# Kernel tuning notes

Measured on AMD Instinct MI355X. Metric: run time of the kernel, lower is better.

The kernel has to match this reference:

```python
import jax, jax.numpy as jnp
import numpy as np

B, C, H, W = 4, 32, 64, 64
K = 3
HEADS = 8
SF = 4
D = C * K * K          # 288, unfold token dim
E = D // 2             # 144, reduced dim
DH = E // HEADS        # 18, head dim
SCALE = DH ** -0.5
N = H * W              # 4096 tokens


def unfold(x):
    # x: (B,C,H,W) -> (B, C*K*K, H*W), torch.nn.Unfold ordering (c, kh, kw)
    xp = jnp.pad(x, ((0, 0), (0, 0), (1, 1), (1, 1)))
    patches = jnp.stack([xp[:, :, i:i + H, j:j + W] for i in range(K) for j in range(K)], axis=2)
    return patches.reshape(x.shape[0], C * K * K, H * W)


def fold(cols):
    # inverse of unfold: scatter-add overlapping patches back, crop padding
    b = cols.shape[0]
    y = cols.reshape(b, C, K, K, H, W)
    out = jnp.zeros((b, C, H + 2, W + 2), cols.dtype)
    for i in range(K):
        for j in range(K):
            out = out.at[:, :, i:i + H, j:j + W].add(y[:, :, i, j])
    return out[:, :, 1:-1, 1:-1]


def layernorm_cols(cols, g, b):
    # LayerNorm over D applied on (B,N,D) view, returned as (B,D,N)
    xt = cols.transpose(0, 2, 1)
    mu = xt.mean(-1, keepdims=True)
    var = xt.var(-1, keepdims=True)
    y = (xt - mu) / jnp.sqrt(var + 1e-5) * g + b
    return y.transpose(0, 2, 1)


def emha(x, wr, br, wqkv, we, be):
    # x: (B, D, N)
    b, _, n_tok = x.shape
    xr = jnp.einsum('bdn,ed->ben', x, wr) + br[None, :, None]   # Conv1d k=1 reduction
    t = xr.transpose(0, 2, 1)                                   # (B,N,E)
    qkv = t @ wqkv.T                                            # Linear, no bias
    q, k, v = jnp.split(qkv, 3, axis=-1)
    n = n_tok // SF

    def rs(a):
        return a.reshape(b, n_tok, HEADS, DH).transpose(0, 2, 1, 3).reshape(b, HEADS, SF, n, DH)

    q, k, v = rs(q), rs(k), rs(v)
    attn = jax.nn.softmax(jnp.einsum('bhsnd,bhsmd->bhsnm', q, k) * SCALE, axis=-1)
    o = jnp.einsum('bhsnm,bhsmd->bhsnd', attn, v)
    o = o.reshape(b, HEADS, n_tok, DH).transpose(0, 2, 1, 3).reshape(b, n_tok, E).transpose(0, 2, 1)
    return jnp.einsum('ben,fe->bfn', o, we) + be[None, :, None]  # Conv1d k=1 expansion


def conv3x3(x, w, b):
    y = jax.lax.conv_general_dilated(x, w, (1, 1), ((1, 1), (1, 1)),
                                     dimension_numbers=('NCHW', 'OIHW', 'NCHW'))
    return y + b[None, :, None, None]


def setup_inputs() -> dict:
    key = jax.random.key(0)
    ks = jax.random.split(key, 20)
    s = 0.02
    inp = {
        'x': jax.random.normal(ks[0], (B, C, H, W), jnp.float32),
        'ln_g': jnp.ones((D,), jnp.float32),
        'ln_b': jnp.zeros((D,), jnp.float32),
        'conv_w': jax.random.normal(ks[1], (C, C, 3, 3), jnp.float32) * s,
        'conv_b': jnp.zeros((C,), jnp.float32),
    }
    for i in range(3):
        k0, k1, k2 = jax.random.split(ks[2 + i], 3)
        inp[f'wr{i+1}'] = jax.random.normal(k0, (E, D), jnp.float32) * s
        inp[f'br{i+1}'] = jnp.zeros((E,), jnp.float32)
        inp[f'wqkv{i+1}'] = jax.random.normal(k1, (3 * E, E), jnp.float32) * s
        inp[f'we{i+1}'] = jax.random.normal(k2, (D, E), jnp.float32) * s
        inp[f'be{i+1}'] = jnp.zeros((D,), jnp.float32)
    return inp


def reference(x, ln_g, ln_b, conv_w, conv_b,
              wr1, br1, wqkv1, we1, be1,
              wr2, br2, wqkv2, we2, be2,
              wr3, br3, wqkv3, we3, be3):
    t = x
    for (wr, br, wqkv, we, be) in ((wr1, br1, wqkv1, we1, be1),
                                   (wr2, br2, wqkv2, we2, be2),
                                   (wr3, br3, wqkv3, we3, be3)):
        cols = unfold(t)
        cols_n = layernorm_cols(cols, ln_g, ln_b)
        cols = emha(cols_n, wr, br, wqkv, we, be) + cols
        t = fold(cols)
    return x + jax.nn.elu(conv3x3(t, conv_w, conv_b))
```

## Files before the change

### kernel.cpp

```cpp
#include <hip/hip_runtime.h>
#include <math.h>

#define BN 4
#define CC 32
#define HH 64
#define WW 64
#define DD 288
#define EE 144
#define NTOK 4096
#define SCALE_F 0.2357022603955158f
#define QSCALE  0.3401074286f
#define QST 192
#define KST 32
#define MQKV 528

typedef __bf16 bf16x8 __attribute__((ext_vector_type(8)));
typedef float floatx4 __attribute__((ext_vector_type(4)));
typedef unsigned short u16x8 __attribute__((ext_vector_type(8)));

__device__ __forceinline__ unsigned short f2bf(float x) {
    unsigned int u = __float_as_uint(x);
    u += 0x7fffu + ((u >> 16) & 1u);
    return (unsigned short)(u >> 16);
}
__device__ __forceinline__ float bf2f(unsigned short s) {
    return __uint_as_float(((unsigned int)s) << 16);
}
__device__ __forceinline__ unsigned int pack_bf_trunc(float a, float b) {
    return __builtin_amdgcn_perm(__float_as_uint(b), __float_as_uint(a), 0x07060302u);
}
__device__ __forceinline__ void plswap32(unsigned int& a, unsigned int& b) {
    asm("v_permlane32_swap_b32 %0, %1" : "+v"(a), "+v"(b));
}
__device__ __forceinline__ void plswap16(unsigned int& a, unsigned int& b) {
    asm("v_permlane16_swap_b32 %0, %1" : "+v"(a), "+v"(b));
}

__global__ __launch_bounds__(256) void setup_k(
    const float* __restrict__ wr0, const float* __restrict__ br0,
    const float* __restrict__ wr1, const float* __restrict__ br1,
    const float* __restrict__ wr2, const float* __restrict__ br2,
    const float* __restrict__ g,  const float* __restrict__ lb,
    const float* __restrict__ wqkv0, const float* __restrict__ wqkv1, const float* __restrict__ wqkv2,
    const float* __restrict__ we0,   const float* __restrict__ we1,   const float* __restrict__ we2,
    unsigned short* __restrict__ wg_bf, float* __restrict__ wgsum, float* __restrict__ wbeta,
    unsigned short* __restrict__ wqkv_bf, unsigned short* __restrict__ we_bf)
{
    int blk = blockIdx.x;
    int tid = threadIdx.x;
    if (blk < 3) {
        if (tid < 144) {
            int l = blk, e = tid;
            const float* wr = (l == 0) ? wr0 : ((l == 1) ? wr1 : wr2);
            const float* br = (l == 0) ? br0 : ((l == 1) ? br1 : br2);
            float sg = 0.f, sb = 0.f;
            for (int d = 0; d < DD; ++d) {
                float w = wr[e * DD + d];
                float wgv = w * g[d];
                wg_bf[((size_t)l * EE + e) * DD + d] = f2bf(wgv);
                sg += wgv;
                sb += w * lb[d];
            }
            wgsum[l * EE + e] = sg;
            wbeta[l * EE + e] = sb + br[e];
        }
        return;
    }
    int idx = (blk - 3) * 256 + tid;
    const int T1 = 3 * MQKV * 160;
    const int T2 = 3 * 288 * 160;
    if (idx < T1) {
        int l = idx / (MQKV * 160), r = idx % (MQKV * 160);
        int m = r / 160, k = r % 160;
        const float* w = (l == 0) ? wqkv0 : ((l == 1) ? wqkv1 : wqkv2);
        float v = 0.f;
        if (k < 144) {
            if (m < 192) {
                int h = m / 24, j = m % 24;
                if (j < 18) v = w[(h * 18 + j) * 144 + k] * QSCALE;
            } else if (m < 384) {
                int mm = m - 192, h = mm / 24, j = mm % 24;
                if (j < 18) v = w[(144 + h * 18 + j) * 144 + k];
            } else {
                v = w[(288 + (m - 384)) * 144 + k];
            }
        }
        wqkv_bf[idx] = f2bf(v);
    } else if (idx < T1 + T2) {
        int j = idx - T1;
        int l = j / (288 * 160), r = j % (288 * 160);
        int m = r / 160, k = r % 160;
        const float* w = (l == 0) ? we0 : ((l == 1) ? we1 : we2);
        we_bf[j] = (k < 144) ? f2bf(w[m * 144 + k]) : 0;
    }
}

__global__ __launch_bounds__(512) void fgemm1_k(
    const float* __restrict__ t, const unsigned short* __restrict__ wg,
    const float* __restrict__ wgsum, const float* __restrict__ wbeta,
    unsigned short* __restrict__ xrT)
{
    __shared__ unsigned short Cs[64 * 296];
    __shared__ float red1[8][64], red2[8][64];
    int tid = threadIdx.x;
    int lane = tid & 63, part = tid >> 6;
    int b = blockIdx.x >> 6, nc = blockIdx.x & 63;
    int w = lane;
    const float* tb = t + (size_t)b * CC * HH * WW;
    __attribute__((aligned(8))) unsigned short loc[36];
    float s1 = 0.f, s2 = 0.f;
    #pragma unroll
    for (int c4 = 0; c4 < 4; ++c4) {
        int c = part * 4 + c4;
        const float* tc = tb + (size_t)c * 4096;
        #pragma unroll
        for (int i = 0; i < 3; ++i) {
            int hr = nc + i - 1;
            bool rok = ((unsigned)hr < 64u);
            #pragma unroll
            for (int j = 0; j < 3; ++j) {
                int wc = w + j - 1;
                bool ok = rok && ((unsigned)wc < 64u);
                float v = ok ? tc[hr * 64 + wc] : 0.f;
                loc[c4 * 9 + i * 3 + j] = f2bf(v);
                s1 += v;
                s2 = fmaf(v, v, s2);
            }
        }
    }
    {
        unsigned short* cr = &Cs[lane * 296 + part * 36];
        #pragma unroll
        for (int k = 0; k < 9; ++k)
            *(unsigned long long*)&cr[k * 4] = *(const unsigned long long*)&loc[k * 4];
    }
    red1[part][lane] = s1;
    red2[part][lane] = s2;
    __syncthreads();
    if (tid < 64) {
        float a = 0.f, q = 0.f;
        #pragma unroll
        for (int p = 0; p < 8; ++p) { a += red1[p][tid]; q += red2[p][tid]; }
        float m = a * (1.f / 288.f);
        float var = q * (1.f / 288.f) - m * m;
        red1[0][tid] = m;
        red2[0][tid] = rsqrtf(var + 1e-5f);
    }
    __syncthreads();

    int l15 = lane & 15, l4 = lane >> 4;
    int tw = part & 3, mh = part >> 2;
    const unsigned short* Ar = wg + (size_t)(mh * 16 + l15) * DD + l4 * 8;
    floatx4 acc[5];
    #pragma unroll
    for (int i = 0; i < 5; ++i) acc[i] = (floatx4){0.f, 0.f, 0.f, 0.f};
    #pragma unroll
    for (int ks = 0; ks < 9; ++ks) {
        bf16x8 bfr = *(const bf16x8*)&Cs[(tw * 16 + l15) * 296 + ks * 32 + l4 * 8];
        #pragma unroll
        for (int i = 0; i < 4; ++i) {
            bf16x8 af = *(const bf16x8*)(Ar + (size_t)i * 32 * DD + ks * 32);
            acc[i] = __builtin_amdgcn_mfma_f32_16x16x32_bf16(af, bfr, acc[i], 0, 0, 0);
        }
        if (mh == 0) {
            bf16x8 af = *(const bf16x8*)(Ar + (size_t)4 * 32 * DD + ks * 32);
            acc[4] = __builtin_amdgcn_mfma_f32_16x16x32_bf16(af, bfr, acc[4], 0, 0, 0);
        }
    }

    __syncthreads();
    {
        int tok = tw * 16 + l15;
        float muv = red1[0][tok], rsv = red2[0][tok];
        #pragma unroll
        for (int i = 0; i < 5; ++i) {
            if (i == 4 && mh) break;
            #pragma unroll
            for (int r = 0; r < 4; ++r) {
                int m = (mh + 2 * i) * 16 + l4 * 4 + r;
                float v = rsv * (acc[i][r] - muv * wgsum[m]) + wbeta[m];
                Cs[tok * 296 + m] = f2bf(v);
            }
        }
    }
    __syncthreads();
    for (int u = tid; u < 64 * 20; u += 512) {
        int row = u / 20, seg = u - row * 20;
        unsigned short* dst = xrT + ((size_t)b * NTOK + nc * 64 + row) * 160 + seg * 8;
        u16x8 val = (seg < 18) ? *(const u16x8*)&Cs[row * 296 + seg * 8] : (u16x8)0;
        *(u16x8*)dst = val;
    }
}

template<int K, int MODE, int NYB>
__global__ __launch_bounds__(256) void mgemm_k(
    const unsigned short* __restrict__ A, const unsigned short* __restrict__ Bt, int BST,
    unsigned short* __restrict__ Ct, unsigned short* __restrict__ Cv, unsigned short* __restrict__ Ck,
    const float* __restrict__ bias)
{
    constexpr int NT = 64;
    __shared__ unsigned short Ts[64 * 56];
    int flat = blockIdx.x;
    int g  = (flat / (8 * NYB)) * 8 + (flat & 7);
    int jm = (flat % (8 * NYB)) >> 3;
    int n0 = (g & 63) * NT;
    int bI = g >> 6;
    int m0 = jm * 48;
    int tid = threadIdx.x;
    int wv = tid >> 6, lane = tid & 63;
    int l15 = lane & 15, l4 = lane >> 4;

    const unsigned short* Arow = A + (size_t)(m0 + l15) * K + l4 * 8;
    const unsigned short* Brow = Bt + ((size_t)bI * NTOK + n0 + wv * 16 + l15) * BST + l4 * 8;

    floatx4 acc[3];
    acc[0] = acc[1] = acc[2] = (floatx4){0.f, 0.f, 0.f, 0.f};

    #pragma unroll
    for (int ks = 0; ks < K / 32; ++ks) {
        bf16x8 bfr = *(const bf16x8*)(Brow + ks * 32);
        #pragma unroll
        for (int mi = 0; mi < 3; ++mi) {
            bf16x8 af = *(const bf16x8*)(Arow + (size_t)mi * 16 * K + ks * 32);
            acc[mi] = __builtin_amdgcn_mfma_f32_16x16x32_bf16(af, bfr, acc[mi], 0, 0, 0);
        }
    }

    int n_l = wv * 16 + l15;

    if (MODE == 2) {
        #pragma unroll
        for (int mi = 0; mi < 3; ++mi)
            #pragma unroll
            for (int r = 0; r < 4; ++r) {
                int m_l = mi * 16 + l4 * 4 + r;
                Ts[m_l * 72 + n_l] = f2bf(acc[mi][r] + bias[m0 + m_l]);
            }
        __syncthreads();
        for (int u = tid; u < 48 * 8; u += 256) {
            int row = u >> 3, seg = u & 7;
            unsigned short* dst = Ct + ((size_t)bI * DD + m0 + row) * NTOK + n0 + seg * 8;
            *(u16x8*)dst = *(const u16x8*)&Ts[row * 72 + seg * 8];
        }
    } else {
        bool vpath = (m0 >= 384);
        #pragma unroll
        for (int mi = 0; mi < 3; ++mi)
            #pragma unroll
            for (int r = 0; r < 4; ++r) {
                int m_l = mi * 16 + l4 * 4 + r;
                float v = acc[mi][r];
                if (!vpath) Ts[n_l * 56 + m_l] = f2bf(v);
                else        Ts[m_l * 72 + n_l] = f2bf(v);
            }
        __syncthreads();
        if (!vpath) {
            if (tid < 128) {
                int row = tid >> 1, half = tid & 1;
                const unsigned short* src = &Ts[row * 56 + half * 24];
                if (m0 >= 192) {
                    int head = (m0 - 192) / 24 + half;
                    unsigned short* dst = Ck + ((size_t)(bI * 8 + head) * NTOK + n0 + row) * KST;
                    #pragma unroll
                    for (int u = 0; u < 3; ++u)
                        *(u16x8*)&dst[u * 8] = *(const u16x8*)&src[u * 8];
                    *(u16x8*)&dst[24] = (u16x8)0;
                } else {
                    unsigned short* dst = Ct + ((size_t)bI * NTOK + n0 + row) * QST + m0 + half * 24;
                    #pragma unroll
                    for (int u = 0; u < 3; ++u)
                        *(u16x8*)&dst[u * 8] = *(const u16x8*)&src[u * 8];
                }
            }
        } else {
            for (int u = tid; u < 48 * 8; u += 256) {
                int row = u >> 3, seg = u & 7;
                unsigned short* dst = Cv + ((size_t)bI * EE + (m0 - 384) + row) * NTOK + n0 + seg * 8;
                *(u16x8*)dst = *(const u16x8*)&Ts[row * 72 + seg * 8];
            }
        }
    }
}

__global__ __launch_bounds__(256, 4) void attn_k2(const unsigned short* __restrict__ qT,
                                                  const unsigned short* __restrict__ kP,
                                                  const unsigned short* __restrict__ vF,
                                                  unsigned short* __restrict__ oT)
{
    int blk = blockIdx.x;
    int bhs = blk & 127;
    int qc  = blk >> 7;
    int b = bhs >> 5, h = (bhs >> 2) & 7, s = bhs & 3;
    int tid  = threadIdx.x;
    int wv   = tid >> 6;
    int lane = tid & 63;
    int l15 = lane & 15, l4 = lane >> 4;
    int q0 = qc * 128;
    int tokbase = s * 1024;

    bf16x8 qf[2];
    #pragma unroll
    for (int ni = 0; ni < 2; ++ni) {
        u16x8 raw = *(const u16x8*)(qT + ((size_t)b * NTOK + tokbase + q0 + wv * 32 + ni * 16 + l15) * QST
                                    + 24 * h + l4 * 8);
        if (l4 == 3) raw = (u16x8)0;
        qf[ni] = *(bf16x8*)&raw;
    }

    floatx4 oacc[2][2];
    #pragma unroll
    for (int ni = 0; ni < 2; ++ni)
        #pragma unroll
        for (int nd = 0; nd < 2; ++nd)
            oacc[ni][nd] = (floatx4){0.f, 0.f, 0.f, 0.f};
    float psum[2] = {0.f, 0.f};

    const unsigned short* kRow = kP + ((size_t)(b * 8 + h) * NTOK + tokbase + l15) * KST + l4 * 8;
    const unsigned short* vRow = vF + ((size_t)b * EE + h * 18) * NTOK + tokbase;

    for (int c0 = 0; c0 < 1024; c0 += 128) {
        #pragma unroll
        for (int sub = 0; sub < 2; ++sub) {
            int base = c0 + sub * 64;
            bf16x8 vfr[2][2];
            #pragma unroll
            for (int c = 0; c < 2; ++c)
                #pragma unroll
                for (int nd = 0; nd < 2; ++nd) {
                    u16x8 raw = *(const u16x8*)(vRow + (size_t)(nd * 16 + l15) * NTOK
                                                + base + c * 32 + l4 * 8);
                    vfr[c][nd] = *(bf16x8*)&raw;
                }
            bf16x8 kf[4];
            #pragma unroll
            for (int mi = 0; mi < 4; ++mi) {
                u16x8 raw = *(const u16x8*)(kRow + (unsigned)(base + mi * 16) * KST);
                kf[mi] = *(bf16x8*)&raw;
            }

            #pragma unroll
            for (int ni = 0; ni < 2; ++ni) {
                floatx4 sacc[4];
                #pragma unroll
                for (int mi = 0; mi < 4; ++mi) {
                    floatx4 z = (floatx4){0.f, 0.f, 0.f, 0.f};
                    sacc[mi] = __builtin_amdgcn_mfma_f32_16x16x32_bf16(kf[mi], qf[ni], z, 0, 0, 0);
                }
                unsigned int pk0[4], pk1[4];
                #pragma unroll
                for (int mi = 0; mi < 4; ++mi) {
                    float e0 = exp2f(sacc[mi][0]), e1 = exp2f(sacc[mi][1]);
                    float e2 = exp2f(sacc[mi][2]), e3 = exp2f(sacc[mi][3]);
                    psum[ni] += (e0 + e1) + (e2 + e3);
                    pk0[mi] = pack_bf_trunc(e0, e1);
                    pk1[mi] = pack_bf_trunc(e2, e3);
                }
                #pragma unroll
                for (int c = 0; c < 2; ++c) {
                    unsigned int B0 = pk0[2 * c], B2 = pk0[2 * c + 1];
                    unsigned int B1 = pk1[2 * c], B3 = pk1[2 * c + 1];
                    plswap32(B0, B2); plswap16(B0, B2);
                    plswap32(B1, B3); plswap16(B1, B3);
                    union { unsigned int u[4]; bf16x8 v; } bfr;
                    bfr.u[0] = B0; bfr.u[1] = B1; bfr.u[2] = B2; bfr.u[3] = B3;
                    #pragma unroll
                    for (int nd = 0; nd < 2; ++nd)
                        oacc[ni][nd] = __builtin_amdgcn_mfma_f32_16x16x32_bf16(vfr[c][nd], bfr.v,
                                                                               oacc[ni][nd], 0, 0, 0);
                }
            }
        }
    }

    #pragma unroll
    for (int ni = 0; ni < 2; ++ni) {
        float p = psum[ni];
        p += __shfl_xor(p, 16, 64);
        p += __shfl_xor(p, 32, 64);
        float inv = 1.f / p;
        size_t rowi = (size_t)b * NTOK + tokbase + q0 + wv * 32 + ni * 16 + l15;
        unsigned short* orow = oT + rowi * 160 + h * 18;
        unsigned int w0 = (unsigned)f2bf(oacc[ni][0][0] * inv) | ((unsigned)f2bf(oacc[ni][0][1] * inv) << 16);
        unsigned int w1 = (unsigned)f2bf(oacc[ni][0][2] * inv) | ((unsigned)f2bf(oacc[ni][0][3] * inv) << 16);
        *(unsigned int*)&orow[l4 * 4]     = w0;
        *(unsigned int*)&orow[l4 * 4 + 2] = w1;
        if (l4 == 0) {
            unsigned int w2 = (unsigned)f2bf(oacc[ni][1][0] * inv) | ((unsigned)f2bf(oacc[ni][1][1] * inv) << 16);
            *(unsigned int*)&orow[16] = w2;
        }
        if (h == 7 && l4 < 2) {
            u16x8 z = (u16x8)0;
            *(u16x8*)(oT + rowi * 160 + 144 + l4 * 8) = z;
        }
    }
}

__global__ __launch_bounds__(256) void fold_k(const unsigned short* __restrict__ cols,
                                              const float* __restrict__ tprev,
                                              float* __restrict__ t)
{
    int idx = blockIdx.x * 256 + threadIdx.x;
    int w = idx & 63;
    int h = (idx >> 6) & 63;
    int c = (idx >> 12) & 31;
    int b = idx >> 17;
    const unsigned short* cb = cols + (size_t)b * DD * NTOK + (size_t)c * 9 * NTOK;
    float sum = 0.f;
    #pragma unroll
    for (int i = 0; i < 3; ++i) {
        int hs = h + 1 - i;
        if ((unsigned)hs < 64u) {
            #pragma unroll
            for (int j = 0; j < 3; ++j) {
                int ws_ = w + 1 - j;
                if ((unsigned)ws_ < 64u)
                    sum += bf2f(cb[(size_t)(i * 3 + j) * NTOK + hs * 64 + ws_]);
            }
        }
    }
    int ch = (h == 0 || h == 63) ? 2 : 3;
    int cw_ = (w == 0 || w == 63) ? 2 : 3;
    t[idx] = sum + (float)(ch * cw_) * tprev[idx];
}

__global__ __launch_bounds__(256) void conv_k(const float* __restrict__ t,
    const float* __restrict__ cw, const float* __restrict__ cbias,
    const float* __restrict__ x, float* __restrict__ out)
{
    __shared__ float wsh[CC * 9];
    int blk = blockIdx.x;
    int band = blk & 3, co = (blk >> 2) & 31, b = blk >> 7;
    int tid = threadIdx.x;
    for (int u = tid; u < CC * 9; u += 256) wsh[u] = cw[co * CC * 9 + u];
    __syncthreads();
    int h = band * 16 + (tid >> 4);
    int w0 = (tid & 15) << 2;
    const float* tb = t + (size_t)b * CC * 4096;
    float bias = cbias[co];
    float a0 = bias, a1 = bias, a2 = bias, a3 = bias;
    for (int ci = 0; ci < CC; ++ci) {
        const float* tc = tb + (size_t)ci * 4096;
        const float* wr = &wsh[ci * 9];
        #pragma unroll
        for (int i = 0; i < 3; ++i) {
            int hr = h + i - 1;
            if ((unsigned)hr < 64u) {
                const float* row = tc + hr * 64;
                float vl = (w0 > 0)  ? row[w0 - 1] : 0.f;
                float4 c4 = *(const float4*)&row[w0];
                float vr = (w0 < 60) ? row[w0 + 4] : 0.f;
                float wj0 = wr[i * 3], wj1 = wr[i * 3 + 1], wj2 = wr[i * 3 + 2];
                a0 = fmaf(wj0, vl,   a0); a0 = fmaf(wj1, c4.x, a0); a0 = fmaf(wj2, c4.y, a0);
                a1 = fmaf(wj0, c4.x, a1); a1 = fmaf(wj1, c4.y, a1); a1 = fmaf(wj2, c4.z, a1);
                a2 = fmaf(wj0, c4.y, a2); a2 = fmaf(wj1, c4.z, a2); a2 = fmaf(wj2, c4.w, a2);
                a3 = fmaf(wj0, c4.z, a3); a3 = fmaf(wj1, c4.w, a3); a3 = fmaf(wj2, vr,   a3);
            }
        }
    }
    size_t oidx = ((size_t)(b * CC + co) * 4096) + h * 64 + w0;
    float4 xin = *(const float4*)&x[oidx];
    float4 o;
    o.x = xin.x + ((a0 > 0.f) ? a0 : (__expf(a0) - 1.f));
    o.y = xin.y + ((a1 > 0.f) ? a1 : (__expf(a1) - 1.f));
    o.z = xin.z + ((a2 > 0.f) ? a2 : (__expf(a2) - 1.f));
    o.w = xin.w + ((a3 > 0.f) ? a3 : (__expf(a3) - 1.f));
    *(float4*)&out[oidx] = o;
}

extern "C" void kernel_launch(void* const* d_in, const int* in_sizes, int n_in,
                              void* d_out, int out_size, void* d_ws, size_t ws_size,
                              hipStream_t stream)
{
    const float* x    = (const float*)d_in[0];
    const float* ln_g = (const float*)d_in[1];
    const float* ln_b = (const float*)d_in[2];
    const float* cw   = (const float*)d_in[3];
    const float* cb   = (const float*)d_in[4];
    const float* wr[3]   = {(const float*)d_in[5],  (const float*)d_in[10], (const float*)d_in[15]};
    const float* br[3]   = {(const float*)d_in[6],  (const float*)d_in[11], (const float*)d_in[16]};
    const float* wqkv[3] = {(const float*)d_in[7],  (const float*)d_in[12], (const float*)d_in[17]};
    const float* we[3]   = {(const float*)d_in[8],  (const float*)d_in[13], (const float*)d_in[18]};
    const float* be[3]   = {(const float*)d_in[9],  (const float*)d_in[14], (const float*)d_in[19]};
    float* out = (float*)d_out;

    char* p = (char*)d_ws;
    unsigned short* cols_bf = (unsigned short*)p; p += (size_t)BN * DD * NTOK * 2;
    unsigned short* oT    = (unsigned short*)p; p += (size_t)BN * NTOK * 288 * 2;
    unsigned short* xrT   = (unsigned short*)p; p += (size_t)BN * NTOK * 160 * 2;
    unsigned short* qT    = (unsigned short*)p; p += (size_t)BN * NTOK * QST * 2;
    unsigned short* kP    = (unsigned short*)p; p += (size_t)BN * 8 * NTOK * KST * 2;
    unsigned short* vF    = (unsigned short*)p; p += (size_t)BN * EE * NTOK * 2;
    float* tA   = (float*)p;              p += (size_t)BN * CC * HH * WW * 4;
    float* tB   = (float*)p;              p += (size_t)BN * CC * HH * WW * 4;
    unsigned short* wg_bf   = (unsigned short*)p; p += (size_t)3 * EE * DD * 2;
    unsigned short* wqkv_bf = (unsigned short*)p; p += (size_t)3 * MQKV * 160 * 2;
    unsigned short* we_bf   = (unsigned short*)p; p += (size_t)3 * DD * 160 * 2;
    float* wgsum = (float*)p;             p += 3 * EE * 4;
    float* wbeta = (float*)p;             p += 3 * EE * 4;
    (void)in_sizes; (void)n_in; (void)out_size; (void)ws_size;

    setup_k<<<1533, 256, 0, stream>>>(wr[0], br[0], wr[1], br[1], wr[2], br[2], ln_g, ln_b,
                                      wqkv[0], wqkv[1], wqkv[2], we[0], we[1], we[2],
                                      wg_bf, wgsum, wbeta, wqkv_bf, we_bf);

    const float* tin = x;
    float* touts[3] = {tA, tB, tA};
    for (int l = 0; l < 3; ++l) {
        fgemm1_k<<<256, 512, 0, stream>>>(tin, wg_bf + (size_t)l * EE * DD,
                                          wgsum + l * EE, wbeta + l * EE, xrT);
        mgemm_k<160, 0, 11><<<2816, 256, 0, stream>>>(
            wqkv_bf + (size_t)l * MQKV * 160, xrT, 160, qT, vF, kP, nullptr);
        attn_k2<<<1024, 256, 0, stream>>>(qT, kP, vF, oT);
        mgemm_k<160, 2, 6><<<1536, 256, 0, stream>>>(
            we_bf + (size_t)l * DD * 160, oT, 160, cols_bf, nullptr, nullptr, be[l]);
        fold_k<<<2048, 256, 0, stream>>>(cols_bf, tin, touts[l]);
        tin = touts[l];
    }
    conv_k<<<512, 256, 0, stream>>>(tA, cw, cb, x, out);
}
```

Before: 452.7 us.

## Stage V tiles in double-buffered LDS and fold softmax row-sum into MFMA

The attention kernel now loads each 128-token V chunk cooperatively into a double-buffered shared-memory tile and prefetches the next chunk and its K fragments into registers while the current chunk computes. This replaces redundant per-wave strided global loads of V. Padding row 31 of the V tile is filled with bf16 ones, so the P·V MFMA also produces the softmax denominator, and the separate exp accumulation and shuffle reduction are dropped. The change adds LDS use, a barrier per chunk and more register pressure from the prefetched K fragments and packed probabilities. The denominator is now summed from bf16-truncated probabilities rather than from fp32 values.

```diff
diff --git a/kernel.cpp b/kernel.cpp
--- a/kernel.cpp
+++ b/kernel.cpp
@@ -287,6 +287,8 @@
                                                   const unsigned short* __restrict__ vF,
                                                   unsigned short* __restrict__ oT)
 {
+    __shared__ unsigned short Vs[2][32 * 136];
+
     int blk = blockIdx.x;
     int bhs = blk & 127;
     int qc  = blk >> 7;
@@ -298,6 +300,14 @@
     int q0 = qc * 128;
     int tokbase = s * 1024;
 
+    for (int v = tid; v < 14 * 16; v += 256) {
+        int d = 18 + (v >> 4), seg = v & 15;
+        unsigned short val = (d == 31) ? (unsigned short)0x3F80 : (unsigned short)0;
+        u16x8 vv = (u16x8)val;
+        *(u16x8*)&Vs[0][d * 136 + seg * 8] = vv;
+        *(u16x8*)&Vs[1][d * 136 + seg * 8] = vv;
+    }
+
     bf16x8 qf[2];
     #pragma unroll
     for (int ni = 0; ni < 2; ++ni) {
@@ -313,71 +323,104 @@
         #pragma unroll
         for (int nd = 0; nd < 2; ++nd)
             oacc[ni][nd] = (floatx4){0.f, 0.f, 0.f, 0.f};
-    float psum[2] = {0.f, 0.f};
+
+    const unsigned short* vbb = vF + (size_t)b * EE * NTOK + tokbase;
+    int d0 = tid >> 4, seg0 = tid & 15;
+    bool x2 = (tid < 32);
+    int d1 = 16 + (tid >> 4), seg1 = tid & 15;
+    const unsigned short* vsrc0 = vbb + (size_t)(h * 18 + d0) * NTOK + seg0 * 8;
+    const unsigned short* vsrc1 = vbb + (size_t)(h * 18 + d1) * NTOK + seg1 * 8;
+
+    {
+        u16x8 v0 = *(const u16x8*)vsrc0;
+        *(u16x8*)&Vs[0][d0 * 136 + seg0 * 8] = v0;
+        if (x2) {
+            u16x8 v1 = *(const u16x8*)vsrc1;
+            *(u16x8*)&Vs[0][d1 * 136 + seg1 * 8] = v1;
+        }
+    }
+    u16x8 pv0 = *(const u16x8*)(vsrc0 + 128);
+    u16x8 pv1;
+    if (x2) pv1 = *(const u16x8*)(vsrc1 + 128);
 
     const unsigned short* kRow = kP + ((size_t)(b * 8 + h) * NTOK + tokbase + l15) * KST + l4 * 8;
-    const unsigned short* vRow = vF + ((size_t)b * EE + h * 18) * NTOK + tokbase;
+    bf16x8 kreg[8];
+    #pragma unroll
+    for (int i = 0; i < 8; ++i) {
+        u16x8 raw = *(const u16x8*)(kRow + (unsigned)(i * 16) * KST);
+        kreg[i] = *(bf16x8*)&raw;
+    }
+    __syncthreads();
 
     for (int c0 = 0; c0 < 1024; c0 += 128) {
-        #pragma unroll
-        for (int sub = 0; sub < 2; ++sub) {
-            int base = c0 + sub * 64;
-            bf16x8 vfr[2][2];
-            #pragma unroll
-            for (int c = 0; c < 2; ++c)
-                #pragma unroll
-                for (int nd = 0; nd < 2; ++nd) {
-                    u16x8 raw = *(const u16x8*)(vRow + (size_t)(nd * 16 + l15) * NTOK
-                                                + base + c * 32 + l4 * 8);
-                    vfr[c][nd] = *(bf16x8*)&raw;
-                }
-            bf16x8 kf[4];
-            #pragma unroll
-            for (int mi = 0; mi < 4; ++mi) {
-                u16x8 raw = *(const u16x8*)(kRow + (unsigned)(base + mi * 16) * KST);
-                kf[mi] = *(bf16x8*)&raw;
-            }
-
+        const int cur = (c0 >> 7) & 1;
+        int cn = c0 + 128;
+        if (cn < 1024) {
+            *(u16x8*)&Vs[cur ^ 1][d0 * 136 + seg0 * 8] = pv0;
+            if (x2) *(u16x8*)&Vs[cur ^ 1][d1 * 136 + seg1 * 8] = pv1;
+            int cn2 = c0 + 256;
+            if (cn2 < 1024) {
+                pv0 = *(const u16x8*)(vsrc0 + cn2);
+                if (x2) pv1 = *(const u16x8*)(vsrc1 + cn2);
+            }
+        }
+
+        unsigned int pk0[2][2][4], pk1[2][2][4];
+        #pragma unroll
+        for (int sub = 0; sub < 2; ++sub)
             #pragma unroll
             for (int ni = 0; ni < 2; ++ni) {
                 floatx4 sacc[4];
                 #pragma unroll
                 for (int mi = 0; mi < 4; ++mi) {
                     floatx4 z = (floatx4){0.f, 0.f, 0.f, 0.f};
-                    sacc[mi] = __builtin_amdgcn_mfma_f32_16x16x32_bf16(kf[mi], qf[ni], z, 0, 0, 0);
+                    sacc[mi] = __builtin_amdgcn_mfma_f32_16x16x32_bf16(kreg[sub * 4 + mi], qf[ni], z, 0, 0, 0);
                 }
-                unsigned int pk0[4], pk1[4];
                 #pragma unroll
                 for (int mi = 0; mi < 4; ++mi) {
-                    float e0 = exp2f(sacc[mi][0]), e1 = exp2f(sacc[mi][1]);
-                    float e2 = exp2f(sacc[mi][2]), e3 = exp2f(sacc[mi][3]);
-                    psum[ni] += (e0 + e1) + (e2 + e3);
-                    pk0[mi] = pack_bf_trunc(e0, e1);
-                    pk1[mi] = pack_bf_trunc(e2, e3);
+                    pk0[sub][ni][mi] = pack_bf_trunc(exp2f(sacc[mi][0]), exp2f(sacc[mi][1]));
+                    pk1[sub][ni][mi] = pack_bf_trunc(exp2f(sacc[mi][2]), exp2f(sacc[mi][3]));
+                }
+            }
+
+        if (cn < 1024) {
+            #pragma unroll
+            for (int i = 0; i < 8; ++i) {
+                u16x8 raw = *(const u16x8*)(kRow + (unsigned)(cn + i * 16) * KST);
+                kreg[i] = *(bf16x8*)&raw;
+            }
+        }
+
+        #pragma unroll
+        for (int sub = 0; sub < 2; ++sub)
+            #pragma unroll
+            for (int c = 0; c < 2; ++c) {
+                union { unsigned int u[4]; bf16x8 v; } bfr[2];
+                #pragma unroll
+                for (int ni = 0; ni < 2; ++ni) {
+                    unsigned int B0 = pk0[sub][ni][2 * c], B2 = pk0[sub][ni][2 * c + 1];
+                    unsigned int B1 = pk1[sub][ni][2 * c], B3 = pk1[sub][ni][2 * c + 1];
+                    plswap32(B0, B2); plswap16(B0, B2);
+                    plswap32(B1, B3); plswap16(B1, B3);
+                    bfr[ni].u[0] = B0; bfr[ni].u[1] = B1; bfr[ni].u[2] = B2; bfr[ni].u[3] = B3;
                 }
                 #pragma unroll
-                for (int c = 0; c < 2; ++c) {
-                    unsigned int B0 = pk0[2 * c], B2 = pk0[2 * c + 1];
-                    unsigned int B1 = pk1[2 * c], B3 = pk1[2 * c + 1];
-                    plswap32(B0, B2); plswap16(B0, B2);
-                    plswap32(B1, B3); plswap16(B1, B3);
-                    union { unsigned int u[4]; bf16x8 v; } bfr;
-                    bfr.u[0] = B0; bfr.u[1] = B1; bfr.u[2] = B2; bfr.u[3] = B3;
+                for (int nd = 0; nd < 2; ++nd) {
+                    bf16x8 af = *(const bf16x8*)&Vs[cur][(nd * 16 + l15) * 136 + sub * 64 + c * 32 + l4 * 8];
                     #pragma unroll
-                    for (int nd = 0; nd < 2; ++nd)
-                        oacc[ni][nd] = __builtin_amdgcn_mfma_f32_16x16x32_bf16(vfr[c][nd], bfr.v,
+                    for (int ni = 0; ni < 2; ++ni)
+                        oacc[ni][nd] = __builtin_amdgcn_mfma_f32_16x16x32_bf16(af, bfr[ni].v,
                                                                                oacc[ni][nd], 0, 0, 0);
                 }
             }
-        }
+
+        __syncthreads();
     }
 
     #pragma unroll
     for (int ni = 0; ni < 2; ++ni) {
-        float p = psum[ni];
-        p += __shfl_xor(p, 16, 64);
-        p += __shfl_xor(p, 32, 64);
-        float inv = 1.f / p;
+        float lsum = __shfl(oacc[ni][1][3], 48 + l15, 64);
+        float inv  = 1.f / lsum;
         size_t rowi = (size_t)b * NTOK + tokbase + q0 + wv * 32 + ni * 16 + l15;
         unsigned short* orow = oT + rowi * 160 + h * 18;
         unsigned int w0 = (unsigned)f2bf(oacc[ni][0][0] * inv) | ((unsigned)f2bf(oacc[ni][0][1] * inv) << 16);
```

New measurement: 452.2 us. Within noise of the previous version (-0.1%).
